# Optimization experiments

Hardware: AMD Instinct MI355X
Metric: run time of the kernel (lower is better)

Reference implementation:

```python
import jax, jax.numpy as jnp
import numpy as np

N = 1_000_000          # points
C_IN = 10              # decorated point features
C_OUT = 64             # pillar feature channels
S = 30_000             # number of pillars (segments)
EPS = 1e-3             # BatchNorm1d eps


def setup_inputs() -> dict:
    key = jax.random.key(0)
    ks = jax.random.split(key, 8)
    inputs = jax.random.normal(ks[0], (N, C_IN), dtype=jnp.float32)
    # every pillar gets ~N/S points; sorted, all segments non-empty
    unq_inv = jnp.sort(jnp.arange(N, dtype=jnp.int32) % S)
    W_lin = jax.random.normal(ks[1], (C_OUT, C_IN), dtype=jnp.float32) * 0.3
    gamma = 1.0 + 0.1 * jax.random.normal(ks[2], (C_OUT,), dtype=jnp.float32)
    beta = 0.1 * jax.random.normal(ks[3], (C_OUT,), dtype=jnp.float32)
    dw1 = jax.random.normal(ks[4], (C_OUT,), dtype=jnp.float32) * 0.5      # depthwise 1x1 conv (groups=C)
    pw1 = jax.random.normal(ks[5], (C_OUT, C_OUT), dtype=jnp.float32) * 0.1  # pointwise 1x1 conv
    dw2 = jax.random.normal(ks[6], (C_OUT,), dtype=jnp.float32) * 0.5
    pw2 = jax.random.normal(ks[7], (C_OUT, C_OUT), dtype=jnp.float32) * 0.1
    return {"inputs": inputs, "unq_inv": unq_inv, "W_lin": W_lin,
            "gamma": gamma, "beta": beta, "dw1": dw1, "pw1": pw1,
            "dw2": dw2, "pw2": pw2}


def reference(inputs, unq_inv, W_lin, gamma, beta, dw1, pw1, dw2, pw2):
    # Linear (no bias) -> BN (training-mode batch stats) -> ReLU
    x = inputs @ W_lin.T                                   # [N, C]
    mu = jnp.mean(x, axis=0)
    var = jnp.mean(jnp.square(x - mu), axis=0)             # biased var, as torch BN
    x = (x - mu) * jax.lax.rsqrt(var + EPS) * gamma + beta
    x = jax.nn.relu(x)

    # MAFF attention: local branch (depthwise scale -> swish -> 1x1 conv)
    s = x * dw1                                            # groups=C 1x1 conv == per-channel scale
    xl = (s * jax.nn.sigmoid(s)) @ pw1.T                   # [N, C]
    # global branch: avg-pool over points -> depthwise scale -> relu -> 1x1 conv
    g = jnp.mean(x, axis=0)                                # [C]
    xg = pw2 @ jax.nn.relu(dw2 * g)                        # [C]
    wei = jax.nn.sigmoid(xl + xg)                          # broadcast [N,C] + [C]
    xi = x * (1.0 + wei)

    # segment reductions keyed by pillar id (scatter_max + scatter_sum)
    x_max = jax.ops.segment_max(xi, unq_inv, num_segments=S,
                                indices_are_sorted=True)
    x_sum = jax.ops.segment_sum(xi, unq_inv, num_segments=S,
                                indices_are_sorted=True)
    return x_max + x_sum                                   # [S, C]
```

## Files before the change

kernel.cpp:

```cpp
#include <hip/hip_runtime.h>
#include <math.h>

#define N_PTS   1000000
#define CI      10
#define C       64
#define NSEG    30000
#define BN_EPS  1e-3f
#define FROFF   31104

#define MSTR 7
#define GOFF 512
#define GSTR 8

using f32x4 = __attribute__((ext_vector_type(4))) float;
using s16x8 = __attribute__((ext_vector_type(8))) short;

__device__ inline short f2bf(float x) {
    unsigned u = __float_as_uint(x);
    unsigned r = (u + 0x7fffu + ((u >> 16) & 1u)) >> 16;
    return (short)r;
}
__device__ inline unsigned pack_trunc(float lo, float hi) {
    return (__float_as_uint(hi) & 0xffff0000u) | (__float_as_uint(lo) >> 16);
}
__device__ inline float frcp(float x) { return __builtin_amdgcn_rcpf(x); }
__device__ inline void lds_fence() {
    asm volatile("s_waitcnt lgkmcnt(0)" ::: "memory");
}

struct Rows { float2 r0, r1, r2, r3; };

__global__ void __launch_bounds__(256) k_moments(const float* __restrict__ inp,
                                                 const int* __restrict__ idx,
                                                 float* __restrict__ ws,
                                                 int* __restrict__ starts) {
    const int tid = threadIdx.x;
    const int stride = gridDim.x * blockDim.x;
    float v[65];
#pragma unroll
    for (int k = 0; k < 65; ++k) v[k] = 0.f;

    int p = blockIdx.x * blockDim.x + tid;
    float2 a0, a1, a2, a3, a4;
    int ic = 0, ip = 0;
    auto ld = [&](int qq) {
        const float2* r2 = (const float2*)(inp + (size_t)qq * CI);
        a0 = r2[0]; a1 = r2[1]; a2 = r2[2]; a3 = r2[3]; a4 = r2[4];
        ic = idx[qq]; ip = (qq > 0) ? idx[qq - 1] : ic;
    };
    if (p < N_PTS) ld(p);
    while (p < N_PTS) {
        float r[CI] = {a0.x, a0.y, a1.x, a1.y, a2.x, a2.y, a3.x, a3.y, a4.x, a4.y};
        const int cc = ic, cp = ip, cq = p;
        const int pn = p + stride;
        if (pn < N_PTS) ld(pn);

#pragma unroll
        for (int i = 0; i < CI; ++i) v[i] += r[i];
        int kk = 10;
#pragma unroll
        for (int i = 0; i < CI; ++i)
#pragma unroll
            for (int j = i; j < CI; ++j) { v[kk] = fmaf(r[i], r[j], v[kk]); ++kk; }

        if (cq == 0) starts[0] = 0;
        else if (cp != cc) starts[cc] = cq;
        p = pn;
    }

#pragma unroll
    for (int k = 0; k < 65; ++k) {
#pragma unroll
        for (int off = 32; off >= 1; off >>= 1)
            v[k] += __shfl_xor(v[k], off, 64);
    }
    __shared__ float red[4 * 65];
    const int wv = tid >> 6, ln = tid & 63;
    if (ln == 0) {
#pragma unroll
        for (int k = 0; k < 65; ++k) red[wv * 65 + k] = v[k];
    }
    __syncthreads();
    if (tid < 65)
        atomicAdd(&ws[MSTR * tid],
                  red[tid] + red[65 + tid] + red[130 + tid] + red[195 + tid]);
}

__global__ void __launch_bounds__(256) k_gstats(const float* __restrict__ inp,
                                                const float* __restrict__ W,
                                                const float* __restrict__ gamma,
                                                const float* __restrict__ beta,
                                                float* __restrict__ ws) {
    const int tid  = threadIdx.x;
    const int wv   = tid >> 6;
    const int lane = tid & 63;
    const int m = lane & 15;
    const int q = lane >> 4;

    __shared__ float wp[C * CI];
    __shared__ float bsh[C];

    if (tid < C) {
        const int c = tid;
        float w[CI];
#pragma unroll
        for (int i = 0; i < CI; ++i) w[i] = W[c * CI + i];
        const float inv_n = 1.f / (float)N_PTS;

        float mu = 0.f;
#pragma unroll
        for (int i = 0; i < CI; ++i) mu = fmaf(w[i], ws[MSTR * i], mu);
        mu *= inv_n;

        float ex2 = 0.f;
        int kk = 10;
#pragma unroll
        for (int i = 0; i < CI; ++i)
#pragma unroll
            for (int j = i; j < CI; ++j) {
                float mm = ws[MSTR * kk];
                float t = w[i] * w[j] * mm;
                ex2 += (i == j) ? t : 2.f * t;
                ++kk;
            }
        ex2 *= inv_n;

        float var = ex2 - mu * mu;
        float rstd = rsqrtf(var + BN_EPS);
        float a = rstd * gamma[c];
        float b = beta[c] - mu * a;
        bsh[c] = b;
#pragma unroll
        for (int i = 0; i < CI; ++i) wp[c * CI + i] = a * w[i];
    }
    __syncthreads();

    s16x8 wfr[4];
#pragma unroll
    for (int nt = 0; nt < 4; ++nt) {
        s16x8 t;
#pragma unroll
        for (int j = 0; j < 8; ++j) {
            int k = 8 * q + j;
            t[j] = (k < CI) ? f2bf(wp[(nt * 16 + m) * CI + k]) : (short)0;
        }
        wfr[nt] = t;
    }
    float bb[4];
#pragma unroll
    for (int nt = 0; nt < 4; ++nt) bb[nt] = bsh[nt * 16 + m];

    const int wid = blockIdx.x * 4 + wv;
    const int nw  = gridDim.x * 4;
    const int NB  = N_PTS / 16;

    auto loadrows = [&](int pb) -> Rows {
        Rows R;
        R.r0 = R.r1 = R.r2 = R.r3 = make_float2(0.f, 0.f);
        const float* row = inp + (size_t)(pb + m) * CI;
        if (q == 0) {
            R.r0 = *(const float2*)(row);     R.r1 = *(const float2*)(row + 2);
            R.r2 = *(const float2*)(row + 4); R.r3 = *(const float2*)(row + 6);
        } else if (q == 1) {
            R.r0 = *(const float2*)(row + 8);
        }
        return R;
    };

    float sm[4] = {0.f, 0.f, 0.f, 0.f};
    const f32x4 zero = {0.f, 0.f, 0.f, 0.f};

    Rows A  = loadrows(wid * 16);
    Rows Bv = loadrows((wid + nw) * 16);
    for (int b = wid; b < NB; b += nw) {
        Rows L = A; A = Bv;
        if (b + 2 * nw < NB) Bv = loadrows((b + 2 * nw) * 16);

        union { s16x8 v; unsigned u[4]; } t;
        t.v = s16x8{0, 0, 0, 0, 0, 0, 0, 0};
        if (q < 2) t.u[0] = pack_trunc(L.r0.x, L.r0.y);
        if (q == 0) {
            t.u[1] = pack_trunc(L.r1.x, L.r1.y);
            t.u[2] = pack_trunc(L.r2.x, L.r2.y);
            t.u[3] = pack_trunc(L.r3.x, L.r3.y);
        }

#pragma unroll
        for (int nt = 0; nt < 4; ++nt) {
            f32x4 xt = __builtin_amdgcn_mfma_f32_16x16x32_bf16(t.v, wfr[nt], zero, 0, 0, 0);
#pragma unroll
            for (int r = 0; r < 4; ++r)
                sm[nt] += fmaxf(xt[r] + bb[nt], 0.f);
        }
    }

#pragma unroll
    for (int nt = 0; nt < 4; ++nt) {
        sm[nt] += __shfl_xor(sm[nt], 16, 64);
        sm[nt] += __shfl_xor(sm[nt], 32, 64);
    }
    float S = sm[0];
    if (q == 1) S = sm[1];
    if (q == 2) S = sm[2];
    if (q == 3) S = sm[3];

    __shared__ float red[4 * 64];
    red[wv * 64 + lane] = S;
    __syncthreads();
    if (tid < 64)
        atomicAdd(&ws[GOFF + GSTR * tid],
                  red[tid] + red[64 + tid] + red[128 + tid] + red[192 + tid]);
}

__global__ void k_prep(const float* __restrict__ W,
                       const float* __restrict__ gamma,
                       const float* __restrict__ beta,
                       const float* __restrict__ dw1,
                       const float* __restrict__ pw1,
                       const float* __restrict__ dw2,
                       const float* __restrict__ pw2,
                       float* __restrict__ ws) {
    const int lane = threadIdx.x;
    const int m = lane & 15, q = lane >> 4;
    const float inv_n = 1.f / (float)N_PTS;

    __shared__ float WP[C * CI];
    __shared__ float BSH[C], T[C], XG[C];

    {
        float w[CI];
#pragma unroll
        for (int i = 0; i < CI; ++i) w[i] = W[lane * CI + i];
        float mu = 0.f;
#pragma unroll
        for (int i = 0; i < CI; ++i) mu = fmaf(w[i], ws[MSTR * i], mu);
        mu *= inv_n;
        float ex2 = 0.f;
        int kk = 10;
#pragma unroll
        for (int i = 0; i < CI; ++i)
#pragma unroll
            for (int j = i; j < CI; ++j) {
                float mm = ws[MSTR * kk];
                float t = w[i] * w[j] * mm;
                ex2 += (i == j) ? t : 2.f * t;
                ++kk;
            }
        ex2 *= inv_n;
        float var = ex2 - mu * mu;
        float rstd = rsqrtf(var + BN_EPS);
        float a = rstd * gamma[lane];
        BSH[lane] = beta[lane] - mu * a;
#pragma unroll
        for (int i = 0; i < CI; ++i) WP[lane * CI + i] = a * w[i];
        T[lane] = fmaxf(dw2[lane] * (ws[GOFF + GSTR * lane] * inv_n), 0.f);
    }
    __syncthreads();

    {
        float acc = 0.f;
#pragma unroll
        for (int k = 0; k < C; ++k) acc = fmaf(pw2[lane * C + k], T[k], acc);
        XG[lane] = acc;
    }
    __syncthreads();

    float4* FR = (float4*)(ws + FROFF);
    union { float4 f; s16x8 v; } u;

#pragma unroll
    for (int nt = 0; nt < 4; ++nt) {
        s16x8 tt;
#pragma unroll
        for (int j = 0; j < 8; ++j) {
            int k = 8 * q + j;
            tt[j] = (k < CI) ? f2bf(WP[(nt * 16 + m) * CI + k]) : (short)0;
        }
        u.v = tt; FR[nt * 64 + lane] = u.f;
    }
#pragma unroll
    for (int nt = 0; nt < 4; ++nt)
#pragma unroll
        for (int kc = 0; kc < 2; ++kc) {
            const float* src = pw1 + (nt * 16 + m) * C + kc * 32 + q * 8;
            float4 p0 = *(const float4*)src, p1 = *(const float4*)(src + 4);
            s16x8 tt;
            tt[0] = f2bf(p0.x); tt[1] = f2bf(p0.y); tt[2] = f2bf(p0.z); tt[3] = f2bf(p0.w);
            tt[4] = f2bf(p1.x); tt[5] = f2bf(p1.y); tt[6] = f2bf(p1.z); tt[7] = f2bf(p1.w);
            u.v = tt; FR[(4 + nt * 2 + kc) * 64 + lane] = u.f;
        }
    float4 f;
    f.x = BSH[m]; f.y = BSH[16 + m]; f.z = BSH[32 + m]; f.w = BSH[48 + m];
    FR[12 * 64 + lane] = f;
    f.x = dw1[m]; f.y = dw1[16 + m]; f.z = dw1[32 + m]; f.w = dw1[48 + m];
    FR[13 * 64 + lane] = f;
    f.x = XG[m]; f.y = XG[16 + m]; f.z = XG[32 + m]; f.w = XG[48 + m];
    FR[14 * 64 + lane] = f;
}

#define LD 68
#define SEGW 2
__global__ void __launch_bounds__(128) k_main(const float* __restrict__ inp,
                                              const float* __restrict__ ws,
                                              const int* __restrict__ starts,
                                              float* __restrict__ out) {
    const int tid  = threadIdx.x;
    const int wv   = tid >> 6;
    const int lane = tid & 63;
    const int m = lane & 15;
    const int q = lane >> 4;
    const f32x4 zero = {0.f, 0.f, 0.f, 0.f};

    const float4* FR = (const float4*)(ws + FROFF);
    union { float4 f; s16x8 v; } u;
    s16x8 wfr[4];
#pragma unroll
    for (int nt = 0; nt < 4; ++nt) { u.f = FR[nt * 64 + lane]; wfr[nt] = u.v; }
    s16x8 bfr[4][2];
#pragma unroll
    for (int nt = 0; nt < 4; ++nt)
#pragma unroll
        for (int kc = 0; kc < 2; ++kc) { u.f = FR[(4 + nt * 2 + kc) * 64 + lane]; bfr[nt][kc] = u.v; }
    const float4 bb4  = FR[12 * 64 + lane];
    const float4 d14  = FR[13 * 64 + lane];
    const float4 xg4  = FR[14 * 64 + lane];
    const float bb[4]  = {bb4.x, bb4.y, bb4.z, bb4.w};
    const float d1v[4] = {d14.x, d14.y, d14.z, d14.w};
    const float xgv[4] = {xg4.x, xg4.y, xg4.z, xg4.w};

    __shared__ float sb[2][2][16 * LD];
    float* t0 = sb[wv][0];
    float* t1 = sb[wv][1];

    const int w  = blockIdx.x * 2 + wv;
    const int s0 = w * SEGW;

    int st1 = starts[s0 + 1];
    int st2 = (s0 + 2 < NSEG) ? starts[s0 + 2] : N_PTS;
    const int start   = starts[s0];
    const int end_all = st2;

    int cur = s0;
    int end_cur = st1;

    float sm[4]  = {0.f, 0.f, 0.f, 0.f};
    float mxv[4] = {-INFINITY, -INFINITY, -INFINITY, -INFINITY};

    auto flushseg = [&](int s) {
#pragma unroll
        for (int nt = 0; nt < 4; ++nt) {
            sm[nt] += __shfl_xor(sm[nt], 16, 64);
            sm[nt] += __shfl_xor(sm[nt], 32, 64);
            mxv[nt] = fmaxf(mxv[nt], __shfl_xor(mxv[nt], 16, 64));
            mxv[nt] = fmaxf(mxv[nt], __shfl_xor(mxv[nt], 32, 64));
        }
        float S = sm[0], M = mxv[0];
        if (q == 1) { S = sm[1]; M = mxv[1]; }
        if (q == 2) { S = sm[2]; M = mxv[2]; }
        if (q == 3) { S = sm[3]; M = mxv[3]; }
        out[(size_t)s * C + lane] = S + M;
#pragma unroll
        for (int nt = 0; nt < 4; ++nt) { sm[nt] = 0.f; mxv[nt] = -INFINITY; }
    };

    auto loadrows = [&](int pb) -> Rows {
        Rows R;
        R.r0 = R.r1 = R.r2 = R.r3 = make_float2(0.f, 0.f);
        const float* row = inp + (size_t)min(pb + m, N_PTS - 1) * CI;
        if (q == 0) {
            R.r0 = *(const float2*)(row);     R.r1 = *(const float2*)(row + 2);
            R.r2 = *(const float2*)(row + 4); R.r3 = *(const float2*)(row + 6);
        } else if (q == 1) {
            R.r0 = *(const float2*)(row + 8);
        }
        return R;
    };

    Rows A0 = loadrows(start);
    Rows A1 = (start + 16 < end_all) ? loadrows(start + 16) : A0;
    Rows B0 = (start + 32 < end_all) ? loadrows(start + 32) : A0;
    Rows B1 = (start + 48 < end_all) ? loadrows(start + 48) : A0;

    auto stage1 = [&](const Rows& L, float* __restrict__ tile, float (&xn)[4][4]) {
        union { s16x8 v; unsigned uu[4]; } t;
        t.v = s16x8{0, 0, 0, 0, 0, 0, 0, 0};
        if (q < 2) t.uu[0] = pack_trunc(L.r0.x, L.r0.y);
        if (q == 0) {
            t.uu[1] = pack_trunc(L.r1.x, L.r1.y);
            t.uu[2] = pack_trunc(L.r2.x, L.r2.y);
            t.uu[3] = pack_trunc(L.r3.x, L.r3.y);
        }
#pragma unroll
        for (int nt = 0; nt < 4; ++nt) {
            f32x4 xt = __builtin_amdgcn_mfma_f32_16x16x32_bf16(t.v, wfr[nt], zero, 0, 0, 0);
#pragma unroll
            for (int r = 0; r < 4; ++r) {
                float x = fmaxf(xt[r] + bb[nt], 0.f);
                xn[nt][r] = x;
                float sg = x * d1v[nt];
                float sw = sg * frcp(1.f + __expf(-sg));
                tile[(4 * q + r) * LD + nt * 16 + m] = sw;
            }
        }
    };

    auto stage2 = [&](const float* __restrict__ tile, const float (&xn)[4][4],
                      f32x4 (&xi)[4]) {
        s16x8 av[2];
#pragma unroll
        for (int kc = 0; kc < 2; ++kc) {
            const float* src = &tile[m * LD + kc * 32 + q * 8];
            float4 p0 = *(const float4*)src;
            float4 p1 = *(const float4*)(src + 4);
            union { s16x8 v; unsigned uu[4]; } tt;
            tt.uu[0] = pack_trunc(p0.x, p0.y);
            tt.uu[1] = pack_trunc(p0.z, p0.w);
            tt.uu[2] = pack_trunc(p1.x, p1.y);
            tt.uu[3] = pack_trunc(p1.z, p1.w);
            av[kc] = tt.v;
        }
#pragma unroll
        for (int nt = 0; nt < 4; ++nt) {
            xi[nt] = __builtin_amdgcn_mfma_f32_16x16x32_bf16(av[0], bfr[nt][0], zero, 0, 0, 0);
            xi[nt] = __builtin_amdgcn_mfma_f32_16x16x32_bf16(av[1], bfr[nt][1], xi[nt], 0, 0, 0);
#pragma unroll
            for (int r = 0; r < 4; ++r) {
                float v   = xi[nt][r] + xgv[nt];
                float wei = frcp(1.f + __expf(-v));
                float x   = xn[nt][r];
                xi[nt][r] = fmaf(x, wei, x);
            }
        }
    };

    auto accum = [&](const f32x4 (&xi)[4], int b16) {
        const int nb = min(16, end_all - b16);
        const int fin = b16 + nb;
        if (fin <= end_cur) {
            if (nb == 16) {
#pragma unroll
                for (int nt = 0; nt < 4; ++nt)
#pragma unroll
                    for (int r = 0; r < 4; ++r) {
                        sm[nt] += xi[nt][r];
                        mxv[nt] = fmaxf(mxv[nt], xi[nt][r]);
                    }
            } else {
#pragma unroll
                for (int nt = 0; nt < 4; ++nt)
#pragma unroll
                    for (int r = 0; r < 4; ++r) {
                        bool act = (4 * q + r) < nb;
                        sm[nt] += act ? xi[nt][r] : 0.f;
                        mxv[nt] = fmaxf(mxv[nt], act ? xi[nt][r] : -INFINITY);
                    }
            }
            if (fin == end_cur) { flushseg(cur); ++cur; end_cur = st2; }
        } else {
            const int B = end_cur - b16;
#pragma unroll
            for (int nt = 0; nt < 4; ++nt)
#pragma unroll
                for (int r = 0; r < 4; ++r) {
                    bool act = (4 * q + r) < B;
                    sm[nt] += act ? xi[nt][r] : 0.f;
                    mxv[nt] = fmaxf(mxv[nt], act ? xi[nt][r] : -INFINITY);
                }
            flushseg(cur); ++cur;
#pragma unroll
            for (int nt = 0; nt < 4; ++nt)
#pragma unroll
                for (int r = 0; r < 4; ++r) {
                    int pt = 4 * q + r;
                    bool act = (pt >= B) && (pt < nb);
                    sm[nt] += act ? xi[nt][r] : 0.f;
                    mxv[nt] = fmaxf(mxv[nt], act ? xi[nt][r] : -INFINITY);
                }
            end_cur = st2;
        }
    };

    for (int base = start; base < end_all; base += 32) {
        Rows L0 = A0, L1 = A1;
        A0 = B0; A1 = B1;
        if (base + 64 < end_all) B0 = loadrows(base + 64);
        if (base + 80 < end_all) B1 = loadrows(base + 80);
        const bool two = (base + 16) < end_all;

        float xn0[4][4], xn1[4][4];
        f32x4 xi0[4], xi1[4];

        stage1(L0, t0, xn0);
        if (two) stage1(L1, t1, xn1);
        lds_fence();

        stage2(t0, xn0, xi0);
        if (two) stage2(t1, xn1, xi1);

        accum(xi0, base);
        if (two) accum(xi1, base + 16);
        lds_fence();
    }
}

extern "C" void kernel_launch(void* const* d_in, const int* in_sizes, int n_in,
                              void* d_out, int out_size, void* d_ws, size_t ws_size,
                              hipStream_t stream) {
    const float* inp   = (const float*)d_in[0];
    const int*   unq   = (const int*)d_in[1];
    const float* W     = (const float*)d_in[2];
    const float* gamma = (const float*)d_in[3];
    const float* beta  = (const float*)d_in[4];
    const float* dw1   = (const float*)d_in[5];
    const float* pw1   = (const float*)d_in[6];
    const float* dw2   = (const float*)d_in[7];
    const float* pw2   = (const float*)d_in[8];
    float* out = (float*)d_out;
    float* ws  = (float*)d_ws;
    int* starts = (int*)ws + 1024;

    hipMemsetAsync(ws, 0, 1024 * sizeof(float), stream);

    k_moments <<<1024, 256, 0, stream>>>(inp, unq, ws, starts);
    k_gstats  <<<1024, 256, 0, stream>>>(inp, W, gamma, beta, ws);
    k_prep    <<<1,    64,  0, stream>>>(W, gamma, beta, dw1, pw1, dw2, pw2, ws);
    k_main    <<<7500, 128, 0, stream>>>(inp, ws, starts, out);
}
```

Baseline: 271.8 us.

## Process four segments per wave with single 16-row tiles and ping-pong LDS

Each wave now handles four pillars instead of two, and the grid is halved to match. The main loop handles one 16-point tile per iteration instead of two. The LDS tile alternates between two buffers, so only one fence per iteration is needed instead of two, and the prefetch depth drops from four tiles to two. This cuts per-wave setup overhead and register pressure, but exposes less instruction-level parallelism per iteration and leaves fewer waves in flight.

After: 264.0 us. -2.8%, faster.

```diff
diff --git a/kernel.cpp b/kernel.cpp
--- a/kernel.cpp
+++ b/kernel.cpp
@@ -299,7 +299,8 @@
 }
 
 #define LD 68
-#define SEGW 2
+#define TILE (16 * LD)
+#define SEGW 4
 __global__ void __launch_bounds__(128) k_main(const float* __restrict__ inp,
                                               const float* __restrict__ ws,
                                               const int* __restrict__ starts,
@@ -328,20 +329,20 @@
     const float d1v[4] = {d14.x, d14.y, d14.z, d14.w};
     const float xgv[4] = {xg4.x, xg4.y, xg4.z, xg4.w};
 
-    __shared__ float sb[2][2][16 * LD];
-    float* t0 = sb[wv][0];
-    float* t1 = sb[wv][1];
+    __shared__ float sb[2][2 * TILE];
+    float* const tbase = sb[wv];
 
     const int w  = blockIdx.x * 2 + wv;
     const int s0 = w * SEGW;
 
-    int st1 = starts[s0 + 1];
-    int st2 = (s0 + 2 < NSEG) ? starts[s0 + 2] : N_PTS;
-    const int start   = starts[s0];
-    const int end_all = st2;
+    const int start = starts[s0];
+    int end_cur = starts[s0 + 1];
+    int n2 = starts[s0 + 2];
+    int n3 = starts[s0 + 3];
+    int n4 = (s0 + 4 < NSEG) ? starts[s0 + 4] : N_PTS;
+    const int end_all = n4;
 
     int cur = s0;
-    int end_cur = st1;
 
     float sm[4]  = {0.f, 0.f, 0.f, 0.f};
     float mxv[4] = {-INFINITY, -INFINITY, -INFINITY, -INFINITY};
@@ -361,6 +362,10 @@
         out[(size_t)s * C + lane] = S + M;
 #pragma unroll
         for (int nt = 0; nt < 4; ++nt) { sm[nt] = 0.f; mxv[nt] = -INFINITY; }
+    };
+
+    auto advance = [&]() {
+        end_cur = n2; n2 = n3; n3 = n4;
     };
 
     auto loadrows = [&](int pb) -> Rows {
@@ -376,12 +381,18 @@
         return R;
     };
 
-    Rows A0 = loadrows(start);
-    Rows A1 = (start + 16 < end_all) ? loadrows(start + 16) : A0;
-    Rows B0 = (start + 32 < end_all) ? loadrows(start + 32) : A0;
-    Rows B1 = (start + 48 < end_all) ? loadrows(start + 48) : A0;
-
-    auto stage1 = [&](const Rows& L, float* __restrict__ tile, float (&xn)[4][4]) {
+    Rows A = loadrows(start);
+    Rows B = (start + 16 < end_all) ? loadrows(start + 16) : A;
+
+    int tog = 0;
+    for (int base = start; base < end_all; base += 16, tog ^= 1) {
+        float* const my = tbase + tog * TILE;
+        Rows L = A;
+        A = B;
+        if (base + 32 < end_all) B = loadrows(base + 32);
+
+        const int nb = min(16, end_all - base);
+
         union { s16x8 v; unsigned uu[4]; } t;
         t.v = s16x8{0, 0, 0, 0, 0, 0, 0, 0};
         if (q < 2) t.uu[0] = pack_trunc(L.r0.x, L.r0.y);
@@ -390,26 +401,29 @@
             t.uu[2] = pack_trunc(L.r2.x, L.r2.y);
             t.uu[3] = pack_trunc(L.r3.x, L.r3.y);
         }
-#pragma unroll
-        for (int nt = 0; nt < 4; ++nt) {
-            f32x4 xt = __builtin_amdgcn_mfma_f32_16x16x32_bf16(t.v, wfr[nt], zero, 0, 0, 0);
+
+        f32x4 xt[4];
+#pragma unroll
+        for (int nt = 0; nt < 4; ++nt)
+            xt[nt] = __builtin_amdgcn_mfma_f32_16x16x32_bf16(t.v, wfr[nt], zero, 0, 0, 0);
+
+        float xn[4][4];
+#pragma unroll
+        for (int nt = 0; nt < 4; ++nt)
 #pragma unroll
             for (int r = 0; r < 4; ++r) {
-                float x = fmaxf(xt[r] + bb[nt], 0.f);
+                float x = fmaxf(xt[nt][r] + bb[nt], 0.f);
                 xn[nt][r] = x;
                 float sg = x * d1v[nt];
                 float sw = sg * frcp(1.f + __expf(-sg));
-                tile[(4 * q + r) * LD + nt * 16 + m] = sw;
+                my[(4 * q + r) * LD + nt * 16 + m] = sw;
             }
-        }
-    };
-
-    auto stage2 = [&](const float* __restrict__ tile, const float (&xn)[4][4],
-                      f32x4 (&xi)[4]) {
+        lds_fence();
+
         s16x8 av[2];
 #pragma unroll
         for (int kc = 0; kc < 2; ++kc) {
-            const float* src = &tile[m * LD + kc * 32 + q * 8];
+            const float* src = &my[m * LD + kc * 32 + q * 8];
             float4 p0 = *(const float4*)src;
             float4 p1 = *(const float4*)(src + 4);
             union { s16x8 v; unsigned uu[4]; } tt;
@@ -419,10 +433,16 @@
             tt.uu[3] = pack_trunc(p1.z, p1.w);
             av[kc] = tt.v;
         }
+
+        f32x4 xi[4];
 #pragma unroll
         for (int nt = 0; nt < 4; ++nt) {
             xi[nt] = __builtin_amdgcn_mfma_f32_16x16x32_bf16(av[0], bfr[nt][0], zero, 0, 0, 0);
             xi[nt] = __builtin_amdgcn_mfma_f32_16x16x32_bf16(av[1], bfr[nt][1], xi[nt], 0, 0, 0);
+        }
+
+#pragma unroll
+        for (int nt = 0; nt < 4; ++nt)
 #pragma unroll
             for (int r = 0; r < 4; ++r) {
                 float v   = xi[nt][r] + xgv[nt];
@@ -430,12 +450,8 @@
                 float x   = xn[nt][r];
                 xi[nt][r] = fmaf(x, wei, x);
             }
-        }
-    };
-
-    auto accum = [&](const f32x4 (&xi)[4], int b16) {
-        const int nb = min(16, end_all - b16);
-        const int fin = b16 + nb;
+
+        const int fin = base + nb;
         if (fin <= end_cur) {
             if (nb == 16) {
 #pragma unroll
@@ -455,14 +471,14 @@
                         mxv[nt] = fmaxf(mxv[nt], act ? xi[nt][r] : -INFINITY);
                     }
             }
-            if (fin == end_cur) { flushseg(cur); ++cur; end_cur = st2; }
+            if (fin == end_cur) { flushseg(cur); ++cur; advance(); }
         } else {
-            const int B = end_cur - b16;
+            const int Bn = end_cur - base;
 #pragma unroll
             for (int nt = 0; nt < 4; ++nt)
 #pragma unroll
                 for (int r = 0; r < 4; ++r) {
-                    bool act = (4 * q + r) < B;
+                    bool act = (4 * q + r) < Bn;
                     sm[nt] += act ? xi[nt][r] : 0.f;
                     mxv[nt] = fmaxf(mxv[nt], act ? xi[nt][r] : -INFINITY);
                 }
@@ -472,34 +488,12 @@
 #pragma unroll
                 for (int r = 0; r < 4; ++r) {
                     int pt = 4 * q + r;
-                    bool act = (pt >= B) && (pt < nb);
+                    bool act = (pt >= Bn) && (pt < nb);
                     sm[nt] += act ? xi[nt][r] : 0.f;
                     mxv[nt] = fmaxf(mxv[nt], act ? xi[nt][r] : -INFINITY);
                 }
-            end_cur = st2;
-        }
-    };
-
-    for (int base = start; base < end_all; base += 32) {
-        Rows L0 = A0, L1 = A1;
-        A0 = B0; A1 = B1;
-        if (base + 64 < end_all) B0 = loadrows(base + 64);
-        if (base + 80 < end_all) B1 = loadrows(base + 80);
-        const bool two = (base + 16) < end_all;
-
-        float xn0[4][4], xn1[4][4];
-        f32x4 xi0[4], xi1[4];
-
-        stage1(L0, t0, xn0);
-        if (two) stage1(L1, t1, xn1);
-        lds_fence();
-
-        stage2(t0, xn0, xi0);
-        if (two) stage2(t1, xn1, xi1);
-
-        accum(xi0, base);
-        if (two) accum(xi1, base + 16);
-        lds_fence();
+            advance();
+        }
     }
 }
 
@@ -524,5 +518,5 @@
     k_moments <<<1024, 256, 0, stream>>>(inp, unq, ws, starts);
     k_gstats  <<<1024, 256, 0, stream>>>(inp, W, gamma, beta, ws);
     k_prep    <<<1,    64,  0, stream>>>(W, gamma, beta, dw1, pw1, dw2, pw2, ws);
-    k_main    <<<7500, 128, 0, stream>>>(inp, ws, starts, out);
-}
+    k_main    <<<3750, 128, 0, stream>>>(inp, ws, starts, out);
+}
```
